# Performance work log

Hardware: AMD Instinct MI355X
Metric: run time of the kernel (lower is better)

The kernel has to match this reference:

```python
import jax, jax.numpy as jnp
import numpy as np

N = 4096       # number of nodes
IN = 512       # input_size
OUT = 256      # output_size
H = 4          # n_heads
HID = OUT // H # per-head hidden = 64
E = 131072     # number of edges (32 * N for full node coverage in edges[0])
NEG_SLOPE = 0.01  # torch nn.LeakyReLU default


def setup_inputs() -> dict:
    key = jax.random.key(0)
    k1, k2, k3, k4 = jax.random.split(key, 4)
    X = jax.random.normal(k1, (N, IN), dtype=jnp.float32)
    edges = jax.random.randint(k2, (2, E), 0, N, dtype=jnp.int32)
    # kaiming_normal_ scale ~ sqrt(2 / fan_in)
    W = jax.random.normal(k3, (IN, OUT), dtype=jnp.float32) * np.sqrt(2.0 / IN).astype(np.float32)
    A = jax.random.normal(k4, (2 * HID, 1), dtype=jnp.float32) * np.sqrt(2.0 / (2 * HID)).astype(np.float32)
    return {"X": X, "edges": edges, "W": W, "A": A}


def reference(X, edges, W, A):
    n = X.shape[0]
    # Faithful to source bug: src, dst = edges[0], edges[0] -> diagonal adjacency
    src = edges[0]
    adj = jnp.zeros((n, n), dtype=bool).at[src, src].set(True)  # [N, N]

    h = (X @ W).reshape(n, H, HID)  # [N, H, HID]

    # e[i, j, h] = leaky_relu( concat(h_i, h_j) . A ) = leaky_relu(a_src[i,h] + a_dst[j,h])
    # (exact decomposition of the original O(N^2 * d) concat @ A)
    a_src = jnp.einsum('nhd,d->nh', h, A[:HID, 0])  # [N, H]
    a_dst = jnp.einsum('nhd,d->nh', h, A[HID:, 0])  # [N, H]
    e = a_src[:, None, :] + a_dst[None, :, :]        # [N, N, H]
    e = jnp.where(e >= 0, e, NEG_SLOPE * e)          # LeakyReLU
    e = jnp.where(adj[:, :, None], e, -jnp.inf)      # mask non-edges

    a = jax.nn.softmax(e, axis=1)                    # softmax over neighbors j
    out = jnp.einsum('ijh,jhf->ihf', a, h)           # [N, H, HID]
    return out.reshape(n, H * HID)
```

## Files before the change

kernel.cpp:

```cpp
#include <hip/hip_runtime.h>

#define N_NODES 4096
#define IN_DIM  512
#define OUT_DIM 256


typedef __attribute__((ext_vector_type(8))) short short8;
typedef __attribute__((ext_vector_type(4))) float floatx4;

#define LDK 520

__device__ inline unsigned int bf_rne(float f) {
    unsigned int u = __float_as_uint(f);
    return u + 0x7fffu + ((u >> 16) & 1u);
}

__device__ inline unsigned int pk_bf16(float lo, float hi) {
    return __builtin_amdgcn_perm(bf_rne(hi), bf_rne(lo), 0x07060302u);
}

__global__ __launch_bounds__(256) void fused_gat_kernel(const float* __restrict__ X,
                                                        const float* __restrict__ W,
                                                        float* __restrict__ out) {
    __shared__ unsigned short Wt[32 * LDK];

    const int tid = threadIdx.x;
    const int r0  = blockIdx.x * 64;
    const int c0  = blockIdx.y * 32;

    {
        const int cc = tid & 7;
        const int kk = tid >> 3;
#pragma unroll
        for (int pass = 0; pass < 8; ++pass) {
            const int k = pass * 64 + kk * 2;
            const float4 w0 = *(const float4*)(W + (size_t)k       * OUT_DIM + c0 + cc * 4);
            const float4 w1 = *(const float4*)(W + (size_t)(k + 1) * OUT_DIM + c0 + cc * 4);
            const float* a0 = (const float*)&w0;
            const float* a1 = (const float*)&w1;
#pragma unroll
            for (int i = 0; i < 4; ++i) {
                *(unsigned int*)&Wt[(cc * 4 + i) * LDK + k] = pk_bf16(a0[i], a1[i]);
            }
        }
    }
    __syncthreads();

    const int lane = tid & 63;
    const int wv   = tid >> 6;
    const int m    = lane & 15;
    const int q    = lane >> 4;

    const float*          xrow = X + (size_t)(r0 + wv * 16 + m) * IN_DIM + q * 8;
    const unsigned short* b0p  = &Wt[(size_t)m        * LDK + q * 8];
    const unsigned short* b1p  = &Wt[(size_t)(m + 16) * LDK + q * 8];

    floatx4 acc0 = {0.f, 0.f, 0.f, 0.f};
    floatx4 acc1 = {0.f, 0.f, 0.f, 0.f};

#pragma unroll
    for (int k = 0; k < IN_DIM; k += 32) {
        const float4 xa = *(const float4*)(xrow + k);
        const float4 xb = *(const float4*)(xrow + k + 4);
        union { unsigned int d[4]; short8 v; } a;
        a.d[0] = pk_bf16(xa.x, xa.y);
        a.d[1] = pk_bf16(xa.z, xa.w);
        a.d[2] = pk_bf16(xb.x, xb.y);
        a.d[3] = pk_bf16(xb.z, xb.w);
        const short8 b0 = *(const short8*)(b0p + k);
        const short8 b1 = *(const short8*)(b1p + k);
        acc0 = __builtin_amdgcn_mfma_f32_16x16x32_bf16(a.v, b0, acc0, 0, 0, 0);
        acc1 = __builtin_amdgcn_mfma_f32_16x16x32_bf16(a.v, b1, acc1, 0, 0, 0);
    }

    float* orow = out + (size_t)(r0 + wv * 16 + q * 4) * OUT_DIM + c0 + m;
#pragma unroll
    for (int i = 0; i < 4; ++i) {
        orow[(size_t)i * OUT_DIM]      = acc0[i];
        orow[(size_t)i * OUT_DIM + 16] = acc1[i];
    }
}

extern "C" void kernel_launch(void* const* d_in, const int* in_sizes, int n_in,
                              void* d_out, int out_size, void* d_ws, size_t ws_size,
                              hipStream_t stream) {
    const float* X = (const float*)d_in[0];
    const float* W = (const float*)d_in[2];
    float* out = (float*)d_out;

    dim3 grid(N_NODES / 64, OUT_DIM / 32);
    fused_gat_kernel<<<grid, 256, 0, stream>>>(X, W, out);
}
```

Measured before the change: 71.31 us.

## Pre-convert X to bf16 in a separate kernel and split GEMM across 8 waves

Adds a pass that converts X to bf16 into workspace once, so the GEMM reads half the bytes and no longer repeats the fp32-to-bf16 conversion in each of the 8 column blocks. The GEMM block grows to 512 threads, each wave computing a single 16x16 output tile instead of two, which doubles per-block parallelism. In exchange it adds a second kernel launch and an extra write and read of the bf16 copy of X.

```diff
diff --git a/kernel.cpp b/kernel.cpp
--- a/kernel.cpp
+++ b/kernel.cpp
@@ -19,29 +19,40 @@
     return __builtin_amdgcn_perm(bf_rne(hi), bf_rne(lo), 0x07060302u);
 }
 
-__global__ __launch_bounds__(256) void fused_gat_kernel(const float* __restrict__ X,
-                                                        const float* __restrict__ W,
-                                                        float* __restrict__ out) {
+__global__ __launch_bounds__(256) void convert_x_kernel(const float* __restrict__ X,
+                                                        unsigned short* __restrict__ Xb) {
+    const size_t i0 = ((size_t)blockIdx.x * 256 + threadIdx.x) * 8;
+    const float4 v0 = *(const float4*)(X + i0);
+    const float4 v1 = *(const float4*)(X + i0 + 4);
+    union { unsigned int d[4]; short8 v; } r;
+    r.d[0] = pk_bf16(v0.x, v0.y);
+    r.d[1] = pk_bf16(v0.z, v0.w);
+    r.d[2] = pk_bf16(v1.x, v1.y);
+    r.d[3] = pk_bf16(v1.z, v1.w);
+    *(short8*)(Xb + i0) = r.v;
+}
+
+__global__ __launch_bounds__(512, 4) void gemm_kernel(const unsigned short* __restrict__ Xb,
+                                                      const float* __restrict__ W,
+                                                      float* __restrict__ out) {
     __shared__ unsigned short Wt[32 * LDK];
 
     const int tid = threadIdx.x;
-    const int r0  = blockIdx.x * 64;
-    const int c0  = blockIdx.y * 32;
+    const int bc0 = blockIdx.y * 32;
 
     {
         const int cc = tid & 7;
-        const int kk = tid >> 3;
+        const int kp = tid >> 3;
 #pragma unroll
-        for (int pass = 0; pass < 8; ++pass) {
-            const int k = pass * 64 + kk * 2;
-            const float4 w0 = *(const float4*)(W + (size_t)k       * OUT_DIM + c0 + cc * 4);
-            const float4 w1 = *(const float4*)(W + (size_t)(k + 1) * OUT_DIM + c0 + cc * 4);
+        for (int pass = 0; pass < 4; ++pass) {
+            const int k = pass * 128 + kp * 2;
+            const float4 w0 = *(const float4*)(W + (size_t)k       * OUT_DIM + bc0 + cc * 4);
+            const float4 w1 = *(const float4*)(W + (size_t)(k + 1) * OUT_DIM + bc0 + cc * 4);
             const float* a0 = (const float*)&w0;
             const float* a1 = (const float*)&w1;
 #pragma unroll
-            for (int i = 0; i < 4; ++i) {
+            for (int i = 0; i < 4; ++i)
                 *(unsigned int*)&Wt[(cc * 4 + i) * LDK + k] = pk_bf16(a0[i], a1[i]);
-            }
         }
     }
     __syncthreads();
@@ -50,35 +61,25 @@
     const int wv   = tid >> 6;
     const int m    = lane & 15;
     const int q    = lane >> 4;
+    const int row  = blockIdx.x * 64 + (wv & 3) * 16 + m;
+    const int cloc = (wv >> 2) * 16;
 
-    const float*          xrow = X + (size_t)(r0 + wv * 16 + m) * IN_DIM + q * 8;
-    const unsigned short* b0p  = &Wt[(size_t)m        * LDK + q * 8];
-    const unsigned short* b1p  = &Wt[(size_t)(m + 16) * LDK + q * 8];
+    const unsigned short* ap = Xb + (size_t)row * IN_DIM + q * 8;
+    const unsigned short* bp = &Wt[(size_t)(cloc + m) * LDK + q * 8];
 
-    floatx4 acc0 = {0.f, 0.f, 0.f, 0.f};
-    floatx4 acc1 = {0.f, 0.f, 0.f, 0.f};
-
+    floatx4 acc = {0.f, 0.f, 0.f, 0.f};
 #pragma unroll
     for (int k = 0; k < IN_DIM; k += 32) {
-        const float4 xa = *(const float4*)(xrow + k);
-        const float4 xb = *(const float4*)(xrow + k + 4);
-        union { unsigned int d[4]; short8 v; } a;
-        a.d[0] = pk_bf16(xa.x, xa.y);
-        a.d[1] = pk_bf16(xa.z, xa.w);
-        a.d[2] = pk_bf16(xb.x, xb.y);
-        a.d[3] = pk_bf16(xb.z, xb.w);
-        const short8 b0 = *(const short8*)(b0p + k);
-        const short8 b1 = *(const short8*)(b1p + k);
-        acc0 = __builtin_amdgcn_mfma_f32_16x16x32_bf16(a.v, b0, acc0, 0, 0, 0);
-        acc1 = __builtin_amdgcn_mfma_f32_16x16x32_bf16(a.v, b1, acc1, 0, 0, 0);
+        const short8 a = *(const short8*)(ap + k);
+        const short8 b = *(const short8*)(bp + k);
+        acc = __builtin_amdgcn_mfma_f32_16x16x32_bf16(a, b, acc, 0, 0, 0);
     }
 
-    float* orow = out + (size_t)(r0 + wv * 16 + q * 4) * OUT_DIM + c0 + m;
+    float* orow = out + (size_t)(blockIdx.x * 64 + (wv & 3) * 16 + q * 4) * OUT_DIM
+                + bc0 + cloc + m;
 #pragma unroll
-    for (int i = 0; i < 4; ++i) {
-        orow[(size_t)i * OUT_DIM]      = acc0[i];
-        orow[(size_t)i * OUT_DIM + 16] = acc1[i];
-    }
+    for (int i = 0; i < 4; ++i)
+        orow[(size_t)i * OUT_DIM] = acc[i];
 }
 
 extern "C" void kernel_launch(void* const* d_in, const int* in_sizes, int n_in,
@@ -88,6 +89,9 @@
     const float* W = (const float*)d_in[2];
     float* out = (float*)d_out;
 
+    unsigned short* Xb = (unsigned short*)d_ws;
+
+    convert_x_kernel<<<(N_NODES * IN_DIM) / (256 * 8), 256, 0, stream>>>(X, Xb);
     dim3 grid(N_NODES / 64, OUT_DIM / 32);
-    fused_gat_kernel<<<grid, 256, 0, stream>>>(X, W, out);
+    gemm_kernel<<<grid, 512, 0, stream>>>(Xb, W, out);
 }
```

After: 73.93 us. 1.04x slower.
